# Kernel tuning notes

Measured on AMD Instinct MI355X. Metric: run time of the kernel, lower is better.

Reference implementation:

```python
import jax, jax.numpy as jnp
import numpy as np

NUM_HEADS = 8
NUM_LAYERS = 4
BASE_THR = 0.5     # AdaptiveLIF base_threshold (state reset -> no adaptation on single step)
TAU_MEM = 5.0      # tau_mem (single step from zero state: mem = decay*0 + x = x)
SURR_SLOPE = 5.0   # fast-sigmoid surrogate slope (forward path unaffected)
EPS = 1e-5
NEG = -1e9


@jax.custom_vjp
def spike(u):
    return (u > 0.0).astype(u.dtype)

def _spike_fwd(u):
    return (u > 0.0).astype(u.dtype), u

def _spike_bwd(u, g):
    return (g / (1.0 + SURR_SLOPE * jnp.abs(u)) ** 2,)

spike.defvjp(_spike_fwd, _spike_bwd)


def lif(x):
    # AdaptiveLIF, single timestep from reset state: mem = x, thr = base_threshold
    return spike(x - BASE_THR)


def layer_norm(x, g, b):
    m = jnp.mean(x, axis=-1, keepdims=True)
    v = jnp.mean((x - m) ** 2, axis=-1, keepdims=True)
    return (x - m) * jax.lax.rsqrt(v + EPS) * g + b


def dsa(x, wq, bq, wk, bk, wv, bv, wo, bo, top_k):
    # Dynamic Sparse Attention: dense scores -> per-query top-k mask -> softmax -> AV
    B, T, D = x.shape
    H = NUM_HEADS
    dh = D // H

    def heads(w, bias):
        return (x @ w.T + bias).reshape(B, T, H, dh).transpose(0, 2, 1, 3)  # [B,H,T,dh]

    q, k, v = heads(wq, bq), heads(wk, bk), heads(wv, bv)
    scores = jnp.einsum('bhqd,bhkd->bhqk', q, k) / jnp.sqrt(jnp.asarray(dh, x.dtype))
    vals, idx = jax.lax.top_k(scores, top_k)  # [B,H,T,K]

    # scatter top-k values into a -inf-filled score matrix (exact top-k sparsity)
    N = B * H * T
    rows = jnp.arange(N)[:, None]
    sp = jnp.full((N, T), NEG, scores.dtype).at[rows, idx.reshape(N, top_k)].set(vals.reshape(N, top_k))
    attn = jax.nn.softmax(sp.reshape(B, H, T, T), axis=-1)

    out = jnp.einsum('bhqk,bhkd->bhqd', attn, v)
    out = out.transpose(0, 2, 1, 3).reshape(B, T, D)
    out = out @ wo.T + bo
    return lif(out)  # spiking output of attention


def ffn(x, w1, b1, w2, b2):
    h = lif(x @ w1.T + b1)
    return lif(h @ w2.T + b2)


def setup_inputs() -> dict:
    key = jax.random.key(0)
    ks = jax.random.split(key, 16)
    L, D, F, IN, OUT, B, T = NUM_LAYERS, 512, 2048, 128, 256, 2, 2048
    s = 0.02
    return {
        'x': jax.random.normal(ks[0], (B, T, IN), jnp.float32),
        'emb_w': jax.random.normal(ks[1], (D, IN), jnp.float32) * s,
        'emb_b': jnp.zeros((D,), jnp.float32),
        'pos_emb': jax.random.normal(ks[2], (1, T, D), jnp.float32) * s,
        'wq': jax.random.normal(ks[3], (L, D, D), jnp.float32) * s,
        'bq': jnp.zeros((L, D), jnp.float32),
        'wk': jax.random.normal(ks[4], (L, D, D), jnp.float32) * s,
        'bk': jnp.zeros((L, D), jnp.float32),
        'wv': jax.random.normal(ks[5], (L, D, D), jnp.float32) * s,
        'bv': jnp.zeros((L, D), jnp.float32),
        'wo': jax.random.normal(ks[6], (L, D, D), jnp.float32) * s,
        'bo': jnp.zeros((L, D), jnp.float32),
        'ln1_g': jnp.ones((L, D), jnp.float32),
        'ln1_b': jnp.zeros((L, D), jnp.float32),
        'fc1_w': jax.random.normal(ks[7], (L, F, D), jnp.float32) * s,
        'fc1_b': jnp.zeros((L, F), jnp.float32),
        'fc2_w': jax.random.normal(ks[8], (L, D, F), jnp.float32) * s,
        'fc2_b': jnp.zeros((L, D), jnp.float32),
        'ln2_g': jnp.ones((L, D), jnp.float32),
        'ln2_b': jnp.zeros((L, D), jnp.float32),
        'fnorm_g': jnp.ones((D,), jnp.float32),
        'fnorm_b': jnp.zeros((D,), jnp.float32),
        'cls_w': jax.random.normal(ks[9], (OUT, D), jnp.float32) * s,
        'cls_b': jnp.zeros((OUT,), jnp.float32),
        'top_k': 32,
    }


def reference(x, emb_w, emb_b, pos_emb, wq, bq, wk, bk, wv, bv, wo, bo,
              ln1_g, ln1_b, fc1_w, fc1_b, fc2_w, fc2_b, ln2_g, ln2_b,
              fnorm_g, fnorm_b, cls_w, cls_b, top_k):
    B, T, _ = x.shape
    h = x @ emb_w.T + emb_b + pos_emb[:, :T, :]
    for l in range(NUM_LAYERS):
        a = dsa(h, wq[l], bq[l], wk[l], bk[l], wv[l], bv[l], wo[l], bo[l], top_k)
        h = layer_norm(h + a, ln1_g[l], ln1_b[l])
        f = ffn(h, fc1_w[l], fc1_b[l], fc2_w[l], fc2_b[l])
        h = layer_norm(h + f, ln2_g[l], ln2_b[l])
    h = layer_norm(h, fnorm_g, fnorm_b)
    pooled = jnp.mean(h, axis=1)  # [B, D]
    return pooled @ cls_w.T + cls_b
```

## Files before the change

### kernel.cpp

```cpp
#include <hip/hip_runtime.h>
#include <math.h>
#include <float.h>

#define T_SEQ  2048
#define DMODEL 512
#define NHEAD  8
#define DHEAD  64
#define FDIM   2048
#define NLAYER 4
#define NB     2
#define MROWS  (NB*T_SEQ)

typedef _Float16 f16x8 __attribute__((ext_vector_type(8)));
typedef float    f32x4 __attribute__((ext_vector_type(4)));

__device__ __forceinline__ void async16(const _Float16* g, _Float16* l) {
    __builtin_amdgcn_global_load_lds(
        (const __attribute__((address_space(1))) unsigned int*)g,
        (__attribute__((address_space(3))) unsigned int*)l, 16, 0, 0);
}

template<int BN, int EPI>
__global__ __launch_bounds__(256) void gemm_k(
    const float* __restrict__ A, const float* __restrict__ W,
    const float* __restrict__ bias, const float* __restrict__ pos,
    float* __restrict__ C, int M, int N, int K)
{
    constexpr int BM = 128;
    constexpr int BK = 32;
    constexpr int MN = BN / 16;
    __shared__ float As[BK][BM + 4];
    __shared__ float Ws[BK][BN + 4];
    const int tid = threadIdx.x;
    const int n0 = blockIdx.x * BN;
    const int m0 = blockIdx.y * BM;
    const int tx = tid & 15;
    const int ty = tid >> 4;

    float acc[8][MN];
    #pragma unroll
    for (int i = 0; i < 8; ++i)
        #pragma unroll
        for (int j = 0; j < MN; ++j) acc[i][j] = 0.f;

    for (int k0 = 0; k0 < K; k0 += BK) {
        #pragma unroll
        for (int it = 0; it < 4; ++it) {
            int qq = tid + 256 * it;
            int m = qq >> 3, kq = qq & 7;
            float4 v4 = *(const float4*)(A + (size_t)(m0 + m) * K + k0 + kq * 4);
            As[kq*4+0][m] = v4.x; As[kq*4+1][m] = v4.y;
            As[kq*4+2][m] = v4.z; As[kq*4+3][m] = v4.w;
        }
        #pragma unroll
        for (int it = 0; it < BN/32; ++it) {
            int qq = tid + 256 * it;
            int n = qq >> 3, kq = qq & 7;
            float4 v4 = *(const float4*)(W + (size_t)(n0 + n) * K + k0 + kq * 4);
            Ws[kq*4+0][n] = v4.x; Ws[kq*4+1][n] = v4.y;
            Ws[kq*4+2][n] = v4.z; Ws[kq*4+3][n] = v4.w;
        }
        __syncthreads();
        for (int kk = 0; kk < BK; ++kk) {
            float a[8], b[MN];
            float4 a0 = *(const float4*)&As[kk][ty*8];
            float4 a1 = *(const float4*)&As[kk][ty*8+4];
            a[0]=a0.x; a[1]=a0.y; a[2]=a0.z; a[3]=a0.w;
            a[4]=a1.x; a[5]=a1.y; a[6]=a1.z; a[7]=a1.w;
            float4 b0 = *(const float4*)&Ws[kk][tx*4];
            b[0]=b0.x; b[1]=b0.y; b[2]=b0.z; b[3]=b0.w;
            if constexpr (MN == 8) {
                float4 b1 = *(const float4*)&Ws[kk][64 + tx*4];
                b[4]=b1.x; b[5]=b1.y; b[6]=b1.z; b[7]=b1.w;
            }
            #pragma unroll
            for (int i = 0; i < 8; ++i)
                #pragma unroll
                for (int j = 0; j < MN; ++j)
                    acc[i][j] = fmaf(a[i], b[j], acc[i][j]);
        }
        __syncthreads();
    }

    #pragma unroll
    for (int i = 0; i < 8; ++i) {
        int m = m0 + ty*8 + i;
        #pragma unroll
        for (int jb = 0; jb < MN/4; ++jb) {
            int nn = n0 + jb*64 + tx*4;
            float4 r;
            r.x = acc[i][jb*4+0] + bias[nn+0];
            r.y = acc[i][jb*4+1] + bias[nn+1];
            r.z = acc[i][jb*4+2] + bias[nn+2];
            r.w = acc[i][jb*4+3] + bias[nn+3];
            if constexpr (EPI == 1) {
                const float* pp = pos + (size_t)(m & (T_SEQ-1)) * DMODEL + nn;
                r.x += pp[0]; r.y += pp[1]; r.z += pp[2]; r.w += pp[3];
            }
            *(float4*)(C + (size_t)m * N + nn) = r;
        }
    }
}

template<int BM, int BN, int ASRC, int EPI, int LAYOUT, int MW>
__global__ __launch_bounds__(512, MW) void mgemm_k(
    const _Float16* __restrict__ AH, const _Float16* __restrict__ AL,
    const _Float16* __restrict__ WH, const _Float16* __restrict__ WL,
    const float* __restrict__ bias,
    float* __restrict__ O0, float* __restrict__ O1, float* __restrict__ O2,
    float* __restrict__ O3, float* __restrict__ O4,
    int M, int N, int K)
{
    constexpr int WMv = (BM == 128) ? 4 : ((BN == 128) ? 2 : 4);
    constexpr int WNv = 8 / WMv;
    constexpr int MI  = BM / WMv / 16;
    constexpr int NJ  = BN / WNv / 16;
    __shared__ _Float16 AsH[2][4][BM][8];
    __shared__ _Float16 AsL[(ASRC == 0) ? 2 : 1][(ASRC == 0) ? 4 : 1][(ASRC == 0) ? BM : 1][8];
    __shared__ _Float16 WsH[2][4][BN][8];
    __shared__ _Float16 WsL[2][4][BN][8];

    const int tid = threadIdx.x;
    const int npan = N / BN;
    const int bid  = blockIdx.x;
    const int n0 = (bid % npan) * BN;
    const int m0 = (bid / npan) * BM;
    const int wv = tid >> 6, lane = tid & 63;
    const int mw = (wv / WNv) * (BM / WMv);
    const int nw = (wv % WNv) * (BN / WNv);
    const int fr = lane & 15;
    const int kb = lane >> 4;

    f16x8 pa0, pal0;

    auto stageW = [&](int k0, int buf) {
        const int kb_ = wv & 3;
        const _Float16* WP = (wv >= 4) ? WL : WH;
        _Float16* db = (wv >= 4) ? &WsL[buf][kb_][0][0] : &WsH[buf][kb_][0][0];
        const size_t sb = ((size_t)((k0 >> 3) + kb_) * N + n0);
        async16(WP + (sb + lane) * 8, db);
        if constexpr (BN == 128)
            async16(WP + (sb + 64 + lane) * 8, db + 64 * 8);
    };
    auto gloadA = [&](int k0) {
        if constexpr (BM == 128) {
            const int r_ = tid >> 2, kb_ = tid & 3;
            pa0 = *(const f16x8*)(AH + (size_t)(m0 + r_) * K + k0 + kb_*8);
            if constexpr (ASRC == 0)
                pal0 = *(const f16x8*)(AL + (size_t)(m0 + r_) * K + k0 + kb_*8);
        } else {
            const int slot = tid & 255, r_ = slot >> 2, kb_ = slot & 3;
            if constexpr (ASRC == 0) {
                const _Float16* src = (tid < 256) ? AH : AL;
                pa0 = *(const f16x8*)(src + (size_t)(m0 + r_) * K + k0 + kb_*8);
            } else {
                if (tid < 256)
                    pa0 = *(const f16x8*)(AH + (size_t)(m0 + r_) * K + k0 + kb_*8);
            }
        }
    };
    auto swriteA = [&](int buf) {
        if constexpr (BM == 128) {
            *(f16x8*)&AsH[buf][tid & 3][tid >> 2][0] = pa0;
            if constexpr (ASRC == 0)
                *(f16x8*)&AsL[buf][tid & 3][tid >> 2][0] = pal0;
        } else {
            const int slot = tid & 255, r_ = slot >> 2, kb_ = slot & 3;
            if constexpr (ASRC == 0) {
                _Float16* d = (tid < 256) ? &AsH[buf][kb_][r_][0] : &AsL[buf][kb_][r_][0];
                *(f16x8*)d = pa0;
            } else {
                if (tid < 256) *(f16x8*)&AsH[buf][kb_][r_][0] = pa0;
            }
        }
    };

    f32x4 acc[MI][NJ];
    #pragma unroll
    for (int i = 0; i < MI; ++i)
        #pragma unroll
        for (int j = 0; j < NJ; ++j) acc[i][j] = (f32x4)(0.f);

    const int NT = K >> 5;
    int cur = 0;
    stageW(0, 0);
    gloadA(0);
    swriteA(0);
    __syncthreads();

    for (int t = 0; t < NT; ++t) {
        const bool more = (t + 1 < NT);
        if (more) {
            stageW((t + 1) << 5, cur ^ 1);
            gloadA((t + 1) << 5);
        }

        f16x8 aH[MI], aL[MI], bH[NJ], bL[NJ];
        #pragma unroll
        for (int i = 0; i < MI; ++i) {
            aH[i] = *(const f16x8*)&AsH[cur][kb][mw + i*16 + fr][0];
            if constexpr (ASRC == 0) aL[i] = *(const f16x8*)&AsL[cur][kb][mw + i*16 + fr][0];
        }
        #pragma unroll
        for (int j = 0; j < NJ; ++j) {
            bH[j] = *(const f16x8*)&WsH[cur][kb][nw + j*16 + fr][0];
            bL[j] = *(const f16x8*)&WsL[cur][kb][nw + j*16 + fr][0];
        }
        #pragma unroll
        for (int i = 0; i < MI; ++i)
            #pragma unroll
            for (int j = 0; j < NJ; ++j) {
                acc[i][j] = __builtin_amdgcn_mfma_f32_16x16x32_f16(aH[i], bH[j], acc[i][j], 0, 0, 0);
                acc[i][j] = __builtin_amdgcn_mfma_f32_16x16x32_f16(aH[i], bL[j], acc[i][j], 0, 0, 0);
                if constexpr (ASRC == 0)
                    acc[i][j] = __builtin_amdgcn_mfma_f32_16x16x32_f16(aL[i], bH[j], acc[i][j], 0, 0, 0);
            }
        if (more) {
            swriteA(cur ^ 1);
            __syncthreads();
            cur ^= 1;
        }
    }

    const int qq = lane >> 4;
    #pragma unroll
    for (int j = 0; j < NJ; ++j) {
        int n = n0 + nw + j*16 + fr;
        float bv = bias[n];
        #pragma unroll
        for (int i = 0; i < MI; ++i) {
            #pragma unroll
            for (int r = 0; r < 4; ++r) {
                int m = m0 + mw + i*16 + qq*4 + r;
                float val = acc[i][j][r] * (1.f/1024.f) + bv;
                if constexpr (EPI == 2) val = val > 0.5f ? 1.f : 0.f;
                if constexpr (EPI == 3) {
                    ((_Float16*)O0)[(size_t)m * N + n] = (val > 0.5f) ? (_Float16)16.f : (_Float16)0.f;
                } else if constexpr (LAYOUT == 0) {
                    O0[(size_t)m * N + n] = val;
                } else {
                    int b_ = m >> 11, t_ = m & (T_SEQ-1);
                    if (n < 512) {
                        size_t hl = (((size_t)(b_*NHEAD + (n>>6))*T_SEQ + t_) << 6) + (n & 63);
                        float s16 = 16.f * val;
                        _Float16 hh = (_Float16)s16;
                        ((_Float16*)O0)[hl] = hh;
                        ((_Float16*)O1)[hl] = (_Float16)(s16 - (float)hh);
                    } else if (n < 1024) {
                        int nn = n - 512;
                        size_t hl = (((size_t)(b_*NHEAD + (nn>>6))*T_SEQ + t_) << 6) + (nn & 63);
                        float s16 = 16.f * val;
                        _Float16 hh = (_Float16)s16;
                        ((_Float16*)O2)[hl] = hh;
                        ((_Float16*)O3)[hl] = (_Float16)(s16 - (float)hh);
                    } else {
                        int nn = n - 1024;
                        O4[(((size_t)(b_*NHEAD + (nn>>6))*T_SEQ + t_) << 6) + (nn & 63)] = val;
                    }
                }
            }
        }
    }
}

__global__ __launch_bounds__(256) void cvtw_k(
    const float* __restrict__ w, _Float16* __restrict__ H, _Float16* __restrict__ L,
    int n, float scale)
{
    int i = blockIdx.x * 256 + threadIdx.x;
    if (i < n) {
        float s = scale * w[i];
        _Float16 h = (_Float16)s;
        H[i] = h;
        L[i] = (_Float16)(s - (float)h);
    }
}

__global__ __launch_bounds__(256) void cvtlayer_k(
    const float* __restrict__ wq, const float* __restrict__ wk, const float* __restrict__ wv,
    const float* __restrict__ bq, const float* __restrict__ bk, const float* __restrict__ bv,
    const float* __restrict__ wo, const float* __restrict__ f1w, const float* __restrict__ f2w,
    _Float16* __restrict__ WcatH, _Float16* __restrict__ WcatL, float* __restrict__ bcat,
    _Float16* __restrict__ WoH, _Float16* __restrict__ WoL,
    _Float16* __restrict__ W1H, _Float16* __restrict__ W1L,
    _Float16* __restrict__ W2H, _Float16* __restrict__ W2L)
{
    int i = blockIdx.x * 256 + threadIdx.x;
    float w;
    _Float16 *H, *L;
    int off;
    if (i < 786432) {
        int j = i;
        int kbq = j / 12288;
        int rem = j - kbq * 12288;
        int n = rem >> 3;
        int k = kbq * 8 + (j & 7);
        int sm = n >> 9, nn = n & 511;
        w = (sm == 0 ? wq : (sm == 1 ? wk : wv))[nn * 512 + k];
        H = WcatH; L = WcatL; off = j;
    } else if (i < 1048576) {
        int j = i - 786432;
        int kbq = j >> 12;
        int n = (j >> 3) & 511;
        int k = (kbq << 3) | (j & 7);
        w = wo[n * 512 + k];
        H = WoH; L = WoL; off = j;
    } else if (i < 2097152) {
        int j = i - 1048576;
        int kbq = j >> 14;
        int n = (j >> 3) & 2047;
        int k = (kbq << 3) | (j & 7);
        w = f1w[n * 512 + k];
        H = W1H; L = W1L; off = j;
    } else if (i < 3145728) {
        int j = i - 2097152;
        int kbq = j >> 12;
        int n = (j >> 3) & 511;
        int k = (kbq << 3) | (j & 7);
        w = f2w[n * 2048 + k];
        H = W2H; L = W2L; off = j;
    } else if (i < 3145728 + 1536) {
        int j = i - 3145728;
        int src = j >> 9, o = j & 511;
        bcat[j] = (src == 0 ? bq : (src == 1 ? bk : bv))[o];
        return;
    } else return;
    float s = 64.f * w;
    _Float16 h = (_Float16)s;
    H[off] = h;
    L[off] = (_Float16)(s - (float)h);
}

__global__ __launch_bounds__(512, 4) void attn_k(
    const _Float16* __restrict__ qH, const _Float16* __restrict__ qL,
    const _Float16* __restrict__ kH, const _Float16* __restrict__ kL,
    const float* __restrict__ v,
    _Float16* __restrict__ outH, _Float16* __restrict__ outL)
{
    __shared__ unsigned char lds[66560];
    _Float16* ksH = (_Float16*)(lds);
    _Float16* ksL = (_Float16*)(lds + 16384);
    float    (*ss)[132] = (float(*)[132])(lds + 32768);
    float*   wrow       = (float*)(lds + 32768);
    int*     irow       = (int*)(lds + 32768 + 8448);

    const int tid = threadIdx.x;
    const int bh  = blockIdx.y;
    const int t0  = blockIdx.x * 64;
    const _Float16* qHb = qH + ((size_t)bh * T_SEQ + t0) * DHEAD;
    const _Float16* qLb = qL + ((size_t)bh * T_SEQ + t0) * DHEAD;
    const _Float16* kHb = kH + (size_t)bh * T_SEQ * DHEAD;
    const _Float16* kLb = kL + (size_t)bh * T_SEQ * DHEAD;
    const float*    vb  = v  + (size_t)bh * T_SEQ * DHEAD;

    unsigned kreg[32];
    #pragma unroll
    for (int i = 0; i < 32; ++i) kreg[i] = 0u;

    const int wv = tid >> 6, lane = tid & 63;
    const int fr = lane & 15, q4 = lane >> 4;
    const int mh  = (wv >> 2) * 32;
    const int c0w = (wv & 3) * 32;
    const int srow = tid >> 3;
    const int ssub = tid & 7;

    f16x8 qaH[2][2], qaL[2][2];
    #pragma unroll
    for (int ks = 0; ks < 2; ++ks) {
        const int doff = ks*32 + q4*8;
        qaH[ks][0] = *(const f16x8*)(qHb + (mh + fr)*DHEAD + doff);
        qaH[ks][1] = *(const f16x8*)(qHb + (mh + 16 + fr)*DHEAD + doff);
        qaL[ks][0] = *(const f16x8*)(qLb + (mh + fr)*DHEAD + doff);
        qaL[ks][1] = *(const f16x8*)(qLb + (mh + 16 + fr)*DHEAD + doff);
    }

    auto stage = [&](int jt) {
        const int j0 = jt * 128;
        #pragma unroll
        for (int i = 0; i < 2; ++i) {
            const int r0 = wv*16 + i*8;
            const int cc = r0 + (lane >> 3);
            const int ch = (lane & 7) ^ (cc & 7);
            const size_t goff = (size_t)(j0 + cc) * DHEAD + ch*8;
            async16(kHb + goff, ksH + r0*64);
            async16(kLb + goff, ksL + r0*64);
        }
    };

    stage(0);
    __syncthreads();

    for (int jt = 0; jt < 16; ++jt) {
        const int j0 = jt * 128;

        f32x4 acc[2][2];
        acc[0][0] = (f32x4)(0.f); acc[0][1] = (f32x4)(0.f);
        acc[1][0] = (f32x4)(0.f); acc[1][1] = (f32x4)(0.f);
        #pragma unroll
        for (int ks = 0; ks < 2; ++ks) {
            const int chq  = ks*4 + q4;
            #pragma unroll
            for (int nj = 0; nj < 2; ++nj) {
                const int cc = c0w + nj*16 + fr;
                const int sl = cc*64 + (chq ^ (cc & 7))*8;
                f16x8 bHf = *(const f16x8*)&ksH[sl];
                f16x8 bLf = *(const f16x8*)&ksL[sl];
                acc[0][nj] = __builtin_amdgcn_mfma_f32_16x16x32_f16(qaH[ks][0], bHf, acc[0][nj], 0, 0, 0);
                acc[0][nj] = __builtin_amdgcn_mfma_f32_16x16x32_f16(qaH[ks][0], bLf, acc[0][nj], 0, 0, 0);
                acc[0][nj] = __builtin_amdgcn_mfma_f32_16x16x32_f16(qaL[ks][0], bHf, acc[0][nj], 0, 0, 0);
                acc[1][nj] = __builtin_amdgcn_mfma_f32_16x16x32_f16(qaH[ks][1], bHf, acc[1][nj], 0, 0, 0);
                acc[1][nj] = __builtin_amdgcn_mfma_f32_16x16x32_f16(qaH[ks][1], bLf, acc[1][nj], 0, 0, 0);
                acc[1][nj] = __builtin_amdgcn_mfma_f32_16x16x32_f16(qaL[ks][1], bHf, acc[1][nj], 0, 0, 0);
            }
        }
        #pragma unroll
        for (int mi = 0; mi < 2; ++mi)
            #pragma unroll
            for (int nj = 0; nj < 2; ++nj)
                #pragma unroll
                for (int r = 0; r < 4; ++r)
                    ss[mh + mi*16 + q4*4 + r][c0w + nj*16 + fr] = acc[mi][nj][r] * (1.f/2048.f);
        __syncthreads();

        if (jt < 15) stage(jt + 1);

        float4 c4[4];
        {
            const float* ssr = &ss[srow][0] + ssub*4;
            #pragma unroll
            for (int g = 0; g < 4; ++g) c4[g] = *(const float4*)(ssr + g*32);
        }
        unsigned cand[16];
        #pragma unroll
        for (int g = 0; g < 4; ++g) {
            float vg[4] = {c4[g].x, c4[g].y, c4[g].z, c4[g].w};
            #pragma unroll
            for (int r = 0; r < 4; ++r) {
                unsigned u = __float_as_uint(vg[r]);
                u ^= (unsigned)((int)u >> 31) | 0x80000000u;
                int col = ssub*4 + g*32 + r;
                cand[g*4+r] = (u & 0xFFFFF800u) | (unsigned)(2047 - (j0 + col));
            }
        }
        #pragma unroll
        for (int k2 = 2; k2 <= 16; k2 <<= 1) {
            #pragma unroll
            for (int j2 = k2 >> 1; j2 > 0; j2 >>= 1) {
                #pragma unroll
                for (int i2 = 0; i2 < 16; ++i2) {
                    int l2 = i2 ^ j2;
                    if (l2 > i2) {
                        unsigned a = cand[i2], b = cand[l2];
                        unsigned mn = a < b ? a : b;
                        unsigned mx = a < b ? b : a;
                        if ((i2 & k2) == 0) { cand[i2] = mx; cand[l2] = mn; }
                        else                { cand[i2] = mn; cand[l2] = mx; }
                    }
                }
            }
        }
        #pragma unroll
        for (int j2 = 0; j2 < 16; ++j2) {
            unsigned b = cand[15 - j2];
            if (kreg[16 + j2] < b) kreg[16 + j2] = b;
        }
        #pragma unroll
        for (int st = 16; st >= 1; st >>= 1) {
            #pragma unroll
            for (int i2 = 0; i2 < 32; ++i2) {
                if ((i2 & st) == 0) {
                    unsigned lo = kreg[i2], hi = kreg[i2 | st];
                    kreg[i2]      = lo < hi ? hi : lo;
                    kreg[i2 | st] = lo < hi ? lo : hi;
                }
            }
        }
        __syncthreads();
    }

    #pragma unroll
    for (int s = 1; s <= 4; s <<= 1) {
        #pragma unroll
        for (int i = 0; i < 16; ++i) {
            unsigned pa = (unsigned)__shfl_xor((int)kreg[31-i], s, 64);
            unsigned pb = (unsigned)__shfl_xor((int)kreg[i],    s, 64);
            if (pa > kreg[i])    kreg[i]    = pa;
            if (pb > kreg[31-i]) kreg[31-i] = pb;
        }
        #pragma unroll
        for (int st = 16; st >= 1; st >>= 1) {
            #pragma unroll
            for (int i2 = 0; i2 < 32; ++i2) {
                if ((i2 & st) == 0) {
                    unsigned lo = kreg[i2], hi = kreg[i2 | st];
                    kreg[i2]      = lo < hi ? hi : lo;
                    kreg[i2 | st] = lo < hi ? lo : hi;
                }
            }
        }
    }

    if (ssub == 0) {
        float w[32];
        #pragma unroll
        for (int i = 0; i < 32; ++i) {
            unsigned um = kreg[i] & 0xFFFFF800u;
            unsigned ub = (um & 0x80000000u) ? (um ^ 0x80000000u) : ~um;
            w[i] = __uint_as_float(ub);
        }
        float m = w[0];
        float s = 0.f;
        #pragma unroll
        for (int i = 0; i < 32; ++i) { w[i] = __expf(w[i] - m); s += w[i]; }
        float inv = 1.f / s;
        #pragma unroll
        for (int i = 0; i < 32; ++i) {
            wrow[srow*33 + i] = w[i] * inv;
            irow[srow*33 + i] = 2047 - (int)(kreg[i] & 0x7FFu);
        }
    }
    __syncthreads();

    const int wid = tid >> 6, lane2 = tid & 63;
    const int b = bh >> 3, h = bh & 7;
    for (int rr = wid; rr < 64; rr += 8) {
        float a0 = 0.f, a1 = 0.f, a2 = 0.f, a3 = 0.f;
        #pragma unroll
        for (int i = 0; i < 8; ++i) {
            a0 = fmaf(wrow[rr*33 + i],      vb[(size_t)irow[rr*33 + i]      * DHEAD + lane2], a0);
            a1 = fmaf(wrow[rr*33 + 8 + i],  vb[(size_t)irow[rr*33 + 8 + i]  * DHEAD + lane2], a1);
            a2 = fmaf(wrow[rr*33 + 16 + i], vb[(size_t)irow[rr*33 + 16 + i] * DHEAD + lane2], a2);
            a3 = fmaf(wrow[rr*33 + 24 + i], vb[(size_t)irow[rr*33 + 24 + i] * DHEAD + lane2], a3);
        }
        float accv = (a0 + a1) + (a2 + a3);
        size_t oi = ((size_t)(b * T_SEQ + t0 + rr)) * DMODEL + h * DHEAD + lane2;
        float s16 = 16.f * accv;
        _Float16 hh = (_Float16)s16;
        outH[oi] = hh;
        outL[oi] = (_Float16)(s16 - (float)hh);
    }
}

__global__ __launch_bounds__(256) void ln_k(
    const float* __restrict__ x, const float* __restrict__ res,
    const float* __restrict__ g, const float* __restrict__ bb,
    float* __restrict__ out, _Float16* __restrict__ oH, _Float16* __restrict__ oL)
{
    __shared__ float red[8];
    const int row = blockIdx.x;
    const int tid = threadIdx.x;
    const float* xr = x + (size_t)row * DMODEL;
    float v0 = xr[tid], v1 = xr[tid + 256];
    if (res) {
        const float* rr = res + (size_t)row * DMODEL;
        v0 += rr[tid]; v1 += rr[tid + 256];
    }
    float s = v0 + v1;
    #pragma unroll
    for (int o = 1; o < 64; o <<= 1) s += __shfl_xor(s, o);
    const int wid = tid >> 6, lane = tid & 63;
    if (lane == 0) red[wid] = s;
    __syncthreads();
    float mean = (red[0] + red[1] + red[2] + red[3]) * (1.f / DMODEL);
    float d0 = v0 - mean, d1 = v1 - mean;
    float qs = d0*d0 + d1*d1;
    #pragma unroll
    for (int o = 1; o < 64; o <<= 1) qs += __shfl_xor(qs, o);
    if (lane == 0) red[4 + wid] = qs;
    __syncthreads();
    float var = (red[4] + red[5] + red[6] + red[7]) * (1.f / DMODEL);
    float rs = rsqrtf(var + 1e-5f);
    float o0 = d0 * rs * g[tid]       + bb[tid];
    float o1 = d1 * rs * g[tid + 256] + bb[tid + 256];
    size_t base = (size_t)row * DMODEL;
    out[base + tid]       = o0;
    out[base + tid + 256] = o1;
    float s0 = 16.f * o0, s1 = 16.f * o1;
    _Float16 h0 = (_Float16)s0, h1 = (_Float16)s1;
    oH[base + tid]       = h0;
    oH[base + tid + 256] = h1;
    oL[base + tid]       = (_Float16)(s0 - (float)h0);
    oL[base + tid + 256] = (_Float16)(s1 - (float)h1);
}

__global__ __launch_bounds__(256) void pool_k(
    const float* __restrict__ h, float* __restrict__ part)
{
    const int chunk = blockIdx.x & 15;
    const int idx = (blockIdx.x >> 4) * 256 + threadIdx.x;
    const int b = idx >> 9, d = idx & 511;
    const float* p = h + ((size_t)b * T_SEQ + chunk * 128) * DMODEL + d;
    float s = 0.f;
    for (int t = 0; t < 128; ++t) s += p[(size_t)t * DMODEL];
    part[chunk * 1024 + idx] = s;
}

__global__ __launch_bounds__(256) void poolsum_k(
    const float* __restrict__ part, float* __restrict__ pooled)
{
    int idx = blockIdx.x * 256 + threadIdx.x;
    float s = 0.f;
    #pragma unroll
    for (int c = 0; c < 16; ++c) s += part[c * 1024 + idx];
    pooled[idx] = s * (1.f / T_SEQ);
}

__global__ __launch_bounds__(256) void cls_k(
    const float* __restrict__ pooled, const float* __restrict__ w,
    const float* __restrict__ bias, float* __restrict__ out)
{
    const int wid = threadIdx.x >> 6, lane = threadIdx.x & 63;
    const int oi = blockIdx.x * 4 + wid;
    const int b = oi >> 8, o = oi & 255;
    const float* pr = pooled + b * DMODEL;
    const float* wr = w + (size_t)o * DMODEL;
    float s = 0.f;
    for (int d = lane; d < DMODEL; d += 64) s = fmaf(pr[d], wr[d], s);
    #pragma unroll
    for (int off = 1; off < 64; off <<= 1) s += __shfl_xor(s, off);
    if (lane == 0) out[oi] = s + bias[o];
}

extern "C" void kernel_launch(void* const* d_in, const int* in_sizes, int n_in,
                              void* d_out, int out_size, void* d_ws, size_t ws_size,
                              hipStream_t stream)
{
    const float* x     = (const float*)d_in[0];
    const float* emb_w = (const float*)d_in[1];
    const float* emb_b = (const float*)d_in[2];
    const float* pos   = (const float*)d_in[3];
    const float* wq    = (const float*)d_in[4];
    const float* bq    = (const float*)d_in[5];
    const float* wk    = (const float*)d_in[6];
    const float* bk    = (const float*)d_in[7];
    const float* wv    = (const float*)d_in[8];
    const float* bv    = (const float*)d_in[9];
    const float* wo    = (const float*)d_in[10];
    const float* bo    = (const float*)d_in[11];
    const float* ln1g  = (const float*)d_in[12];
    const float* ln1b  = (const float*)d_in[13];
    const float* fc1w  = (const float*)d_in[14];
    const float* fc1b  = (const float*)d_in[15];
    const float* fc2w  = (const float*)d_in[16];
    const float* fc2b  = (const float*)d_in[17];
    const float* ln2g  = (const float*)d_in[18];
    const float* ln2b  = (const float*)d_in[19];
    const float* fng   = (const float*)d_in[20];
    const float* fnb   = (const float*)d_in[21];
    const float* clsw  = (const float*)d_in[22];
    const float* clsb  = (const float*)d_in[23];

    float* ws = (float*)d_ws;
    const size_t SZ  = (size_t)MROWS * DMODEL;
    const size_t HP  = SZ / 2;
    float*     h     = ws;
    float*     t1    = ws + 1*SZ;
    _Float16*  hH    = (_Float16*)(ws + 2*SZ);
    _Float16*  hL    = (_Float16*)(ws + 2*SZ + HP);
    _Float16*  aoH   = (_Float16*)(ws + 3*SZ);
    _Float16*  aoL   = (_Float16*)(ws + 3*SZ + HP);
    _Float16*  qbH   = (_Float16*)(ws + 4*SZ);
    _Float16*  qbL   = (_Float16*)(ws + 4*SZ + HP);
    _Float16*  kbH   = (_Float16*)(ws + 5*SZ);
    _Float16*  kbL   = (_Float16*)(ws + 5*SZ + HP);
    float*     vbuf  = ws + 6*SZ;
    _Float16*  WcatH = (_Float16*)(ws + 7*SZ);
    _Float16*  WcatL = (_Float16*)(ws + 7*SZ + 393216);
    _Float16*  WoH   = (_Float16*)(ws + 7*SZ + 786432);
    _Float16*  WoL   = (_Float16*)(ws + 7*SZ + 917504);
    _Float16*  W1H   = (_Float16*)(ws + 7*SZ + 1048576);
    _Float16*  W1L   = (_Float16*)(ws + 7*SZ + 1572864);
    _Float16*  W2H   = (_Float16*)(ws + 7*SZ + 2097152);
    _Float16*  W2L   = (_Float16*)(ws + 7*SZ + 2621440);
    float*     bcat  = ws + 7*SZ + 3145728;
    float*     pooled= ws + 7*SZ + 3145728 + 1536;
    float*     part  = ws + 7*SZ + 3145728 + 1536 + 1024;
    _Float16*  hid   = (_Float16*)(ws + 4*SZ);
    const size_t needed = (7*SZ + 3145728 + 1536 + 1024 + 16384) * sizeof(float);
    if (ws_size < needed) return;

    dim3 blk(256);

    gemm_k<64,1><<<dim3(DMODEL/64, MROWS/128), blk, 0, stream>>>(
        x, emb_w, emb_b, pos, h, MROWS, DMODEL, 128);
    cvtw_k<<<dim3((int)(SZ/256)), blk, 0, stream>>>(h, hH, hL, (int)SZ, 16.f);

    for (int l = 0; l < NLAYER; ++l) {
        const float* wq_l = wq + (size_t)l*DMODEL*DMODEL;
        const float* bq_l = bq + (size_t)l*DMODEL;
        const float* wk_l = wk + (size_t)l*DMODEL*DMODEL;
        const float* bk_l = bk + (size_t)l*DMODEL;
        const float* wv_l = wv + (size_t)l*DMODEL*DMODEL;
        const float* bv_l = bv + (size_t)l*DMODEL;
        const float* wo_l = wo + (size_t)l*DMODEL*DMODEL;
        const float* bo_l = bo + (size_t)l*DMODEL;
        const float* f1w_l = fc1w + (size_t)l*FDIM*DMODEL;
        const float* f1b_l = fc1b + (size_t)l*FDIM;
        const float* f2w_l = fc2w + (size_t)l*DMODEL*FDIM;
        const float* f2b_l = fc2b + (size_t)l*DMODEL;

        cvtlayer_k<<<dim3(12294), blk, 0, stream>>>(
            wq_l, wk_l, wv_l, bq_l, bk_l, bv_l, wo_l, f1w_l, f2w_l,
            WcatH, WcatL, bcat, WoH, WoL, W1H, W1L, W2H, W2L);

        mgemm_k<64,128,0,0,2,6><<<dim3(768), dim3(512), 0, stream>>>(
            hH, hL, WcatH, WcatL, bcat,
            (float*)qbH, (float*)qbL, (float*)kbH, (float*)kbL, vbuf,
            MROWS, 1536, DMODEL);

        attn_k<<<dim3(T_SEQ/64, NB*NHEAD), dim3(512), 0, stream>>>(
            qbH, qbL, kbH, kbL, vbuf, aoH, aoL);

        mgemm_k<64,64,0,2,0,4><<<dim3(512), dim3(512), 0, stream>>>(
            aoH, aoL, WoH, WoL, bo_l, t1, nullptr, nullptr, nullptr, nullptr,
            MROWS, DMODEL, DMODEL);
        ln_k<<<dim3(MROWS), blk, 0, stream>>>(h, t1, ln1g + (size_t)l*DMODEL,
                                              ln1b + (size_t)l*DMODEL, h, hH, hL);

        mgemm_k<128,128,0,3,0,4><<<dim3(512), dim3(512), 0, stream>>>(
            hH, hL, W1H, W1L, f1b_l, (float*)hid, nullptr, nullptr, nullptr, nullptr,
            MROWS, FDIM, DMODEL);
        mgemm_k<64,64,1,2,0,4><<<dim3(512), dim3(512), 0, stream>>>(
            hid, nullptr, W2H, W2L, f2b_l, t1, nullptr, nullptr, nullptr, nullptr,
            MROWS, DMODEL, FDIM);
        ln_k<<<dim3(MROWS), blk, 0, stream>>>(h, t1, ln2g + (size_t)l*DMODEL,
                                              ln2b + (size_t)l*DMODEL, h, hH, hL);
    }

    ln_k<<<dim3(MROWS), blk, 0, stream>>>(h, nullptr, fng, fnb, h, hH, hL);
    pool_k<<<dim3(64), blk, 0, stream>>>(h, part);
    poolsum_k<<<dim3(4), blk, 0, stream>>>(part, pooled);
    cls_k<<<dim3(128), blk, 0, stream>>>(pooled, clsw, clsb, (float*)d_out);
}
```

Baseline: 1.062 ms.

## Stage GEMM A operand via async global-to-LDS loads using k-blocked activation layout

Activation producers (embedding conversion, attention output, layernorm, FFN spike epilogue) now write fp16 hi/lo operands in a k-block-major [K/8][M][8] layout instead of row-major. The GEMM then loads its A tiles with async global_load_lds, just as it already did for weights, replacing the register load plus LDS write. This removes the register round-trip and the separate LDS store before the barrier. The cost is strided, scattered 2-byte stores in the producer kernels, and correctness depends on every producer of A matching the new layout.

Measured after the change: 1.073 ms. No clear change (+1.0%).

```diff
diff --git a/kernel.cpp b/kernel.cpp
--- a/kernel.cpp
+++ b/kernel.cpp
@@ -131,46 +131,31 @@
     const int fr = lane & 15;
     const int kb = lane >> 4;
 
-    f16x8 pa0, pal0;
-
-    auto stageW = [&](int k0, int buf) {
+    auto stage = [&](int k0, int buf) {
         const int kb_ = wv & 3;
-        const _Float16* WP = (wv >= 4) ? WL : WH;
-        _Float16* db = (wv >= 4) ? &WsL[buf][kb_][0][0] : &WsH[buf][kb_][0][0];
-        const size_t sb = ((size_t)((k0 >> 3) + kb_) * N + n0);
-        async16(WP + (sb + lane) * 8, db);
-        if constexpr (BN == 128)
-            async16(WP + (sb + 64 + lane) * 8, db + 64 * 8);
-    };
-    auto gloadA = [&](int k0) {
-        if constexpr (BM == 128) {
-            const int r_ = tid >> 2, kb_ = tid & 3;
-            pa0 = *(const f16x8*)(AH + (size_t)(m0 + r_) * K + k0 + kb_*8);
-            if constexpr (ASRC == 0)
-                pal0 = *(const f16x8*)(AL + (size_t)(m0 + r_) * K + k0 + kb_*8);
-        } else {
-            const int slot = tid & 255, r_ = slot >> 2, kb_ = slot & 3;
+        {
+            const _Float16* WP = (wv >= 4) ? WL : WH;
+            _Float16* db = (wv >= 4) ? &WsL[buf][kb_][0][0] : &WsH[buf][kb_][0][0];
+            const size_t sb = ((size_t)((k0 >> 3) + kb_) * N + n0);
+            async16(WP + (sb + lane) * 8, db);
+            if constexpr (BN == 128)
+                async16(WP + (sb + 64 + lane) * 8, db + 64 * 8);
+        }
+        {
+            const size_t sb = ((size_t)((k0 >> 3) + kb_) * M + m0);
             if constexpr (ASRC == 0) {
-                const _Float16* src = (tid < 256) ? AH : AL;
-                pa0 = *(const f16x8*)(src + (size_t)(m0 + r_) * K + k0 + kb_*8);
+                const _Float16* AP = (wv >= 4) ? AL : AH;
+                _Float16* db = (wv >= 4) ? &AsL[buf][kb_][0][0] : &AsH[buf][kb_][0][0];
+                async16(AP + (sb + lane) * 8, db);
+                if constexpr (BM == 128)
+                    async16(AP + (sb + 64 + lane) * 8, db + 64 * 8);
             } else {
-                if (tid < 256)
-                    pa0 = *(const f16x8*)(AH + (size_t)(m0 + r_) * K + k0 + kb_*8);
-            }
-        }
-    };
-    auto swriteA = [&](int buf) {
-        if constexpr (BM == 128) {
-            *(f16x8*)&AsH[buf][tid & 3][tid >> 2][0] = pa0;
-            if constexpr (ASRC == 0)
-                *(f16x8*)&AsL[buf][tid & 3][tid >> 2][0] = pal0;
-        } else {
-            const int slot = tid & 255, r_ = slot >> 2, kb_ = slot & 3;
-            if constexpr (ASRC == 0) {
-                _Float16* d = (tid < 256) ? &AsH[buf][kb_][r_][0] : &AsL[buf][kb_][r_][0];
-                *(f16x8*)d = pa0;
-            } else {
-                if (tid < 256) *(f16x8*)&AsH[buf][kb_][r_][0] = pa0;
+                if (wv < 4) {
+                    _Float16* db = &AsH[buf][kb_][0][0];
+                    async16(AH + (sb + lane) * 8, db);
+                    if constexpr (BM == 128)
+                        async16(AH + (sb + 64 + lane) * 8, db + 64 * 8);
+                }
             }
         }
     };
@@ -183,17 +168,12 @@
 
     const int NT = K >> 5;
     int cur = 0;
-    stageW(0, 0);
-    gloadA(0);
-    swriteA(0);
+    stage(0, 0);
     __syncthreads();
 
     for (int t = 0; t < NT; ++t) {
         const bool more = (t + 1 < NT);
-        if (more) {
-            stageW((t + 1) << 5, cur ^ 1);
-            gloadA((t + 1) << 5);
-        }
+        if (more) stage((t + 1) << 5, cur ^ 1);
 
         f16x8 aH[MI], aL[MI], bH[NJ], bL[NJ];
         #pragma unroll
@@ -216,7 +196,6 @@
                     acc[i][j] = __builtin_amdgcn_mfma_f32_16x16x32_f16(aL[i], bH[j], acc[i][j], 0, 0, 0);
             }
         if (more) {
-            swriteA(cur ^ 1);
             __syncthreads();
             cur ^= 1;
         }
@@ -235,7 +214,8 @@
                 float val = acc[i][j][r] * (1.f/1024.f) + bv;
                 if constexpr (EPI == 2) val = val > 0.5f ? 1.f : 0.f;
                 if constexpr (EPI == 3) {
-                    ((_Float16*)O0)[(size_t)m * N + n] = (val > 0.5f) ? (_Float16)16.f : (_Float16)0.f;
+                    ((_Float16*)O0)[(((size_t)(n >> 3)) * M + m) * 8 + (n & 7)] =
+                        (val > 0.5f) ? (_Float16)16.f : (_Float16)0.f;
                 } else if constexpr (LAYOUT == 0) {
                     O0[(size_t)m * N + n] = val;
                 } else {
@@ -271,8 +251,10 @@
     if (i < n) {
         float s = scale * w[i];
         _Float16 h = (_Float16)s;
-        H[i] = h;
-        L[i] = (_Float16)(s - (float)h);
+        int m = i >> 9, c = i & 511;
+        size_t d = (((size_t)(c >> 3)) * MROWS + m) * 8 + (c & 7);
+        H[d] = h;
+        L[d] = (_Float16)(s - (float)h);
     }
 }
 
@@ -533,7 +515,9 @@
             a3 = fmaf(wrow[rr*33 + 24 + i], vb[(size_t)irow[rr*33 + 24 + i] * DHEAD + lane2], a3);
         }
         float accv = (a0 + a1) + (a2 + a3);
-        size_t oi = ((size_t)(b * T_SEQ + t0 + rr)) * DMODEL + h * DHEAD + lane2;
+        int col = h * DHEAD + lane2;
+        size_t rowg = (size_t)(b * T_SEQ + t0 + rr);
+        size_t oi = (((size_t)(col >> 3)) * MROWS + rowg) * 8 + (col & 7);
         float s16 = 16.f * accv;
         _Float16 hh = (_Float16)s16;
         outH[oi] = hh;
@@ -577,10 +561,12 @@
     out[base + tid + 256] = o1;
     float s0 = 16.f * o0, s1 = 16.f * o1;
     _Float16 h0 = (_Float16)s0, h1 = (_Float16)s1;
-    oH[base + tid]       = h0;
-    oH[base + tid + 256] = h1;
-    oL[base + tid]       = (_Float16)(s0 - (float)h0);
-    oL[base + tid + 256] = (_Float16)(s1 - (float)h1);
+    size_t d0i = (((size_t)(tid >> 3)) * MROWS + row) * 8 + (tid & 7);
+    size_t d1i = (((size_t)((tid + 256) >> 3)) * MROWS + row) * 8 + (tid & 7);
+    oH[d0i] = h0;
+    oH[d1i] = h1;
+    oL[d0i] = (_Float16)(s0 - (float)h0);
+    oL[d1i] = (_Float16)(s1 - (float)h1);
 }
 
 __global__ __launch_bounds__(256) void pool_k(
```

## Load weight fragments directly from global into registers, bypassing LDS staging

Applied to the files above, without the earlier changes.

Removes the LDS staging buffers for the hi/lo weight panels in the split-fp16 MFMA GEMM, so each wave loads its B fragments straight from global memory into registers. When per-wave fragments are small, it double-buffers them in registers and alternates two A LDS buffers in a manually unrolled loop. Otherwise it loads the weights synchronously each step. This cuts LDS traffic and footprint, which may help occupancy, but weight reuse across waves now depends on cache hits rather than shared memory, and the non-double-buffered path exposes global load latency.

After: 1.109 ms. 4.5% more time.

```diff
diff --git a/kernel.cpp b/kernel.cpp
--- a/kernel.cpp
+++ b/kernel.cpp
@@ -117,8 +117,6 @@
     constexpr int NJ  = BN / WNv / 16;
     __shared__ _Float16 AsH[2][4][BM][8];
     __shared__ _Float16 AsL[(ASRC == 0) ? 2 : 1][(ASRC == 0) ? 4 : 1][(ASRC == 0) ? BM : 1][8];
-    __shared__ _Float16 WsH[2][4][BN][8];
-    __shared__ _Float16 WsL[2][4][BN][8];
 
     const int tid = threadIdx.x;
     const int npan = N / BN;
@@ -133,15 +131,6 @@
 
     f16x8 pa0, pal0;
 
-    auto stageW = [&](int k0, int buf) {
-        const int kb_ = wv & 3;
-        const _Float16* WP = (wv >= 4) ? WL : WH;
-        _Float16* db = (wv >= 4) ? &WsL[buf][kb_][0][0] : &WsH[buf][kb_][0][0];
-        const size_t sb = ((size_t)((k0 >> 3) + kb_) * N + n0);
-        async16(WP + (sb + lane) * 8, db);
-        if constexpr (BN == 128)
-            async16(WP + (sb + 64 + lane) * 8, db + 64 * 8);
-    };
     auto gloadA = [&](int k0) {
         if constexpr (BM == 128) {
             const int r_ = tid >> 2, kb_ = tid & 3;
@@ -175,36 +164,29 @@
         }
     };
 
+    auto loadW = [&](int k0, f16x8 (&dH)[NJ], f16x8 (&dL)[NJ]) {
+        const size_t kk = ((size_t)(k0 >> 3) + kb) * N;
+        #pragma unroll
+        for (int j = 0; j < NJ; ++j) {
+            const size_t off = (kk + n0 + nw + j*16 + fr) * 8;
+            dH[j] = *(const f16x8*)(WH + off);
+            dL[j] = *(const f16x8*)(WL + off);
+        }
+    };
+
     f32x4 acc[MI][NJ];
     #pragma unroll
     for (int i = 0; i < MI; ++i)
         #pragma unroll
         for (int j = 0; j < NJ; ++j) acc[i][j] = (f32x4)(0.f);
 
-    const int NT = K >> 5;
-    int cur = 0;
-    stageW(0, 0);
-    gloadA(0);
-    swriteA(0);
-    __syncthreads();
-
-    for (int t = 0; t < NT; ++t) {
-        const bool more = (t + 1 < NT);
-        if (more) {
-            stageW((t + 1) << 5, cur ^ 1);
-            gloadA((t + 1) << 5);
-        }
-
-        f16x8 aH[MI], aL[MI], bH[NJ], bL[NJ];
+    auto mfma_step = [&](int buf, f16x8 (&bH)[NJ], f16x8 (&bL)[NJ]) {
+        f16x8 aH[MI], aL[MI];
         #pragma unroll
         for (int i = 0; i < MI; ++i) {
-            aH[i] = *(const f16x8*)&AsH[cur][kb][mw + i*16 + fr][0];
-            if constexpr (ASRC == 0) aL[i] = *(const f16x8*)&AsL[cur][kb][mw + i*16 + fr][0];
-        }
-        #pragma unroll
-        for (int j = 0; j < NJ; ++j) {
-            bH[j] = *(const f16x8*)&WsH[cur][kb][nw + j*16 + fr][0];
-            bL[j] = *(const f16x8*)&WsL[cur][kb][nw + j*16 + fr][0];
+            aH[i] = *(const f16x8*)&AsH[buf][kb][mw + i*16 + fr][0];
+            if constexpr (ASRC == 0)
+                aL[i] = *(const f16x8*)&AsL[buf][kb][mw + i*16 + fr][0];
         }
         #pragma unroll
         for (int i = 0; i < MI; ++i)
@@ -215,10 +197,39 @@
                 if constexpr (ASRC == 0)
                     acc[i][j] = __builtin_amdgcn_mfma_f32_16x16x32_f16(aL[i], bH[j], acc[i][j], 0, 0, 0);
             }
-        if (more) {
-            swriteA(cur ^ 1);
-            __syncthreads();
-            cur ^= 1;
+    };
+
+    const int NT = K >> 5;
+    constexpr bool WDB = (NJ <= 2) && (MW <= 4);
+    f16x8 bAH[NJ], bAL[NJ];
+
+    if constexpr (WDB) {
+        f16x8 bBH[NJ], bBL[NJ];
+        loadW(0, bAH, bAL);
+        gloadA(0); swriteA(0);
+        __syncthreads();
+        for (int t = 0; t < NT; t += 2) {
+            if (t + 1 < NT) { loadW((t+1) << 5, bBH, bBL); gloadA((t+1) << 5); }
+            mfma_step(0, bAH, bAL);
+            if (t + 1 < NT) { swriteA(1); __syncthreads(); }
+            if (t + 2 < NT) { loadW((t+2) << 5, bAH, bAL); gloadA((t+2) << 5); }
+            if (t + 1 < NT) mfma_step(1, bBH, bBL);
+            if (t + 2 < NT) { swriteA(0); __syncthreads(); }
+        }
+    } else {
+        int cur = 0;
+        gloadA(0); swriteA(0);
+        __syncthreads();
+        for (int t = 0; t < NT; ++t) {
+            const bool more = (t + 1 < NT);
+            if (more) gloadA((t + 1) << 5);
+            loadW(t << 5, bAH, bAL);
+            mfma_step(cur, bAH, bAL);
+            if (more) {
+                swriteA(cur ^ 1);
+                __syncthreads();
+                cur ^= 1;
+            }
         }
     }
 
```
